# Kernel tuning notes

Measured on AMD Instinct MI355X. Metric: run time of the kernel, lower is better.

The kernel has to match this reference:

```python
import jax, jax.numpy as jnp
import numpy as np
from jax.scipy.linalg import expm

N_WIRES = 9
N_LAYERS = 4
EMBED = 512
BATCH = 64
D = 2 ** N_WIRES
P = N_WIRES * N_LAYERS * 2  # gate angles per sample


def _apply_gate(st, g, w):
    # st: (D, 2,...,2) complex64; apply 2x2 gate g on wire w
    st = jnp.moveaxis(st, 1 + w, -1)
    st = st @ g.T  # new[a] = sum_b g[a,b] old[b]
    return jnp.moveaxis(st, -1, 1 + w)


def _apply_cnot(st, c, t):
    st = jnp.moveaxis(st, (1 + c, 1 + t), (-2, -1))
    st = jnp.concatenate([st[..., 0:1, :], st[..., 1:2, ::-1]], axis=-2)
    return jnp.moveaxis(st, (-2, -1), (1 + c, 1 + t))


def _build_unitary(params):
    # simulate circuit on all D basis states at once (identity input)
    st = jnp.eye(D, dtype=jnp.complex64).reshape((D,) + (2,) * N_WIRES)
    idx = 0
    for _ in range(N_LAYERS):
        for w in range(N_WIRES):
            thy = params[idx]
            thz = params[idx + 1]
            idx += 2
            c = jnp.cos(thy * 0.5).astype(jnp.complex64)
            s = jnp.sin(thy * 0.5).astype(jnp.complex64)
            ry = jnp.stack([jnp.stack([c, -s]), jnp.stack([s, c])])
            ep = jnp.exp(0.5j * thz.astype(jnp.complex64))  # exp(i*thz/2)
            zero = jnp.zeros((), jnp.complex64)
            rz = jnp.stack([jnp.stack([jnp.conj(ep), zero]), jnp.stack([zero, ep])])
            st = _apply_gate(st, rz @ ry, w)  # Ry then Rz, fused
        for w in range(N_WIRES - 1):
            st = _apply_cnot(st, w, w + 1)
        st = _apply_cnot(st, N_WIRES - 1, 0)  # ring entangler (n_wires>1)
    # row index = input basis state i -> column i of U; take real part
    return jnp.real(st.reshape(D, D)).T


def _forward(t, w1, b1, w2, b2):
    h = jax.nn.silu(t[:, None] @ w1 + b1)          # (B, EMBED)
    params = h @ w2 + b2                            # (B, P)
    p_sg = jax.lax.stop_gradient(params)            # torch uses .detach() for the circuit
    U_stack = jax.vmap(_build_unitary)(p_sg)        # (B, D, D)
    B = t.shape[0]
    A = jnp.zeros((B, D * D), params.dtype).at[:, :P].set(params).reshape(B, D, D)
    A_skew = (A - jnp.swapaxes(A, -1, -2)) * 0.01
    U_diff = jax.vmap(expm)(A_skew)                 # (B, D, D)
    return jnp.einsum('bij,bjk->bik', U_stack, U_diff)


def setup_inputs() -> dict:
    key = jax.random.key(0)
    k_t, k1, kb1, k2, kb2 = jax.random.split(key, 5)
    t = jax.random.normal(k_t, (BATCH,), jnp.float32)
    w1 = jax.random.normal(k1, (1, EMBED), jnp.float32)
    b1 = jax.random.normal(kb1, (EMBED,), jnp.float32) * 0.1
    w2 = jax.random.normal(k2, (EMBED, P), jnp.float32) / np.sqrt(EMBED)
    b2 = jax.random.normal(kb2, (P,), jnp.float32) * 0.1
    return {"t": t, "w1": w1, "b1": b1, "w2": w2, "b2": b2}


def reference(t, w1, b1, w2, b2):
    return _forward(t, w1, b1, w2, b2)
```

## Files before the change

### kernel.cpp

```cpp
#include <hip/hip_runtime.h>
#include <math.h>


#define PSTRIDE 2560
#define GD_OFF  0
#define SC_OFF  144
#define L_OFF(l) (160 + (l)*256)
#define V_OFF   1184
#define W_OFF   1280
#define C0_OFF  1792

__device__ __forceinline__ float2 cmul(float2 a, float2 b){
  return make_float2(fmaf(a.x, b.x, -a.y*b.y), fmaf(a.x, b.y, a.y*b.x));
}

__device__ __forceinline__ float2 pk_fma_s_lo(float2 s2, float2 b, float2 c){
  float2 d;
  asm("v_pk_fma_f32 %0, %1, %2, %3 op_sel:[0,0,0] op_sel_hi:[0,1,1]"
      : "=v"(d) : "s"(s2), "v"(b), "v"(c));
  return d;
}
__device__ __forceinline__ float2 pk_mul_s_hi(float2 s2, float2 b){
  float2 d;
  asm("v_pk_mul_f32 %0, %1, %2 op_sel:[1,0] op_sel_hi:[1,1]"
      : "=v"(d) : "s"(s2), "v"(b));
  return d;
}
__device__ __forceinline__ float2 pk_fma_vs_lo(float2 a, float2 b, float2 c){
  float2 d;
  asm("v_pk_fma_f32 %0, %1, %2, %3 op_sel:[0,0,0] op_sel_hi:[0,1,1]"
      : "=v"(d) : "v"(a), "s"(b), "v"(c));
  return d;
}
__device__ __forceinline__ float2 pk_mul_vs_hi(float2 a, float2 b){
  float2 d;
  asm("v_pk_mul_f32 %0, %1, %2 op_sel:[1,0] op_sel_hi:[1,1]"
      : "=v"(d) : "v"(a), "s"(b));
  return d;
}
__device__ __forceinline__ float2 pk_fma_vv_lo(float2 a, float2 b, float2 c){
  float2 d;
  asm("v_pk_fma_f32 %0, %1, %2, %3 op_sel:[0,0,0] op_sel_hi:[0,1,1]"
      : "=v"(d) : "v"(a), "v"(b), "v"(c));
  return d;
}
__device__ __forceinline__ float2 pk_mul_vv_hi(float2 a, float2 b){
  float2 d;
  asm("v_pk_mul_f32 %0, %1, %2 op_sel:[1,0] op_sel_hi:[1,1]"
      : "=v"(d) : "v"(a), "v"(b));
  return d;
}
__device__ __forceinline__ float2 pk_swapneg(float2 c, float2 n){
  float2 d;
  asm("v_pk_mul_f32 %0, %1, %2 op_sel:[1,0] op_sel_hi:[0,1]"
      : "=v"(d) : "v"(c), "v"(n));
  return d;
}

__device__ __forceinline__ int Fperm(int x){
  int S = x ^ (x >> 1); S ^= S >> 2; S ^= S >> 4; S ^= S >> 8;
  return (S & 0xFF) | ((((x >> 8) ^ S) & 1) << 8);
}
__device__ __forceinline__ int physmap(int x){ return x ^ ((x >> 4) & 15); }

template<int STRIDE, bool UNIF>
__device__ __forceinline__ void apply_rot(float2 amp[8], const float* rp){
  const float2 R0 = ((const float2*)rp)[0];
  const float2 R1 = ((const float2*)rp)[1];
  #pragma unroll
  for (int b = 0; b < 8; ++b){
    if (b & STRIDE) continue;
    const float2 u = amp[b], v = amp[b + STRIDE];
    if constexpr (UNIF){
      amp[b]          = pk_fma_s_lo(R0, u, pk_mul_s_hi(R0, v));
      amp[b + STRIDE] = pk_fma_s_lo(R1, u, pk_mul_s_hi(R1, v));
    } else {
      amp[b]          = pk_fma_vv_lo(R0, u, pk_mul_vv_hi(R0, v));
      amp[b + STRIDE] = pk_fma_vv_lo(R1, u, pk_mul_vv_hi(R1, v));
    }
  }
}

template<bool UNIF>
__device__ __forceinline__ void run_layer(float2* __restrict__ S,
    const float* __restrict__ lb, const int lane,
    const int base1, const int base2, const int base3, const int baseF,
    const float2 NEG1P1){
  float2 amp[8];
  #pragma unroll
  for (int j = 0; j < 8; ++j) amp[j] = S[base1 ^ j];
  apply_rot<4, UNIF>(amp, lb + 6*4);
  apply_rot<2, UNIF>(amp, lb + 7*4);
  apply_rot<1, UNIF>(amp, lb + 8*4);
  #pragma unroll
  for (int j = 0; j < 8; ++j) S[base1 ^ j] = amp[j];
  #pragma unroll
  for (int j = 0; j < 8; ++j) amp[j] = S[base2 ^ ((j << 3) ^ (j >> 1))];
  apply_rot<4, UNIF>(amp, lb + 3*4);
  apply_rot<2, UNIF>(amp, lb + 4*4);
  apply_rot<1, UNIF>(amp, lb + 5*4);
  #pragma unroll
  for (int j = 0; j < 8; ++j) S[base2 ^ ((j << 3) ^ (j >> 1))] = amp[j];
  #pragma unroll
  for (int j = 0; j < 8; ++j) amp[j] = S[base3 ^ ((j << 6) ^ ((4*j) & 15))];
  apply_rot<4, UNIF>(amp, lb + 0*4);
  apply_rot<2, UNIF>(amp, lb + 1*4);
  apply_rot<1, UNIF>(amp, lb + 2*4);
  {
    const float2 A  = *(const float2*)(lb + 128 + lane*2);
    const float2 A2 = pk_swapneg(A, NEG1P1);
    #pragma unroll
    for (int j = 0; j < 8; ++j)
      amp[j] = pk_fma_vv_lo(amp[j], A, pk_mul_vv_hi(amp[j], A2));
    #pragma unroll
    for (int j = 0; j < 8; ++j){
      const float2 P = *(const float2*)(lb + 64 + j*4);
      const float2 Q = *(const float2*)(lb + 64 + j*4 + 2);
      if constexpr (UNIF)
        amp[j] = pk_fma_vs_lo(amp[j], P, pk_mul_vs_hi(amp[j], Q));
      else
        amp[j] = pk_fma_vv_lo(amp[j], P, pk_mul_vv_hi(amp[j], Q));
    }
  }
  #pragma unroll
  for (int j = 0; j < 8; ++j) S[baseF ^ physmap(Fperm(j << 6))] = amp[j];
}

__global__ __launch_bounds__(576)
void prep_kernel(const float* __restrict__ t,  const float* __restrict__ w1,
                 const float* __restrict__ b1, const float* __restrict__ w2,
                 const float* __restrict__ b2, float* __restrict__ prep){
  __shared__ float sh[512];
  __shared__ float part[8][72];
  __shared__ float spar[72];
  __shared__ float tl[4][256];
  __shared__ float ssc[3];
  __shared__ __align__(16) float2 vst[2][512];
  const int s = blockIdx.x;
  const float ts = t[s];
  for (int k = threadIdx.x; k < 512; k += 576){
    const float z = fmaf(ts, w1[k], b1[k]);
    sh[k] = z / (1.f + expf(-z));
  }
  __syncthreads();
  {
    const int p = threadIdx.x % 72, c = threadIdx.x / 72;
    float acc = 0.f;
    const int k0 = c*64;
    for (int k = k0; k < k0 + 64; ++k) acc = fmaf(sh[k], w2[k*72 + p], acc);
    part[c][p] = acc;
  }
  __syncthreads();
  if (threadIdx.x < 72){
    const int p = threadIdx.x;
    float acc = b2[p];
    #pragma unroll
    for (int c = 0; c < 8; ++c) acc += part[c][p];
    spar[p] = acc;
  }
  __syncthreads();
  float* pb = prep + (size_t)s*PSTRIDE;
  const int tid = threadIdx.x;
  if (tid < 256){
    const int l = tid >> 6, m = tid & 63;
    float2 acc = make_float2(1.f, 0.f);
    #pragma unroll
    for (int w = 3; w < 9; ++w){
      const float thz = spar[2*(9*l + w) + 1];
      float zi, zr; sincosf(0.5f*thz, &zi, &zr);
      const int bit = (m >> (8 - w)) & 1;
      acc = cmul(acc, make_float2(zr, bit ? zi : -zi));
    }
    pb[L_OFF(l) + 128 + 2*m]     = acc.x;
    pb[L_OFF(l) + 128 + 2*m + 1] = acc.y;
    tl[l][128 + 2*m]     = acc.x;
    tl[l][128 + 2*m + 1] = acc.y;
  } else if (tid < 288){
    const int q = tid - 256, l = q >> 3, j = q & 7;
    float2 acc = make_float2(1.f, 0.f);
    #pragma unroll
    for (int w = 0; w < 3; ++w){
      const float thz = spar[2*(9*l + w) + 1];
      float zi, zr; sincosf(0.5f*thz, &zi, &zr);
      const int bit = (j >> (2 - w)) & 1;
      acc = cmul(acc, make_float2(zr, bit ? zi : -zi));
    }
    float* o = pb + L_OFF(l) + 64 + j*4;
    o[0] = acc.x; o[1] = acc.y; o[2] = -acc.y; o[3] = acc.x;
    float* o2 = &tl[l][64 + j*4];
    o2[0] = acc.x; o2[1] = acc.y; o2[2] = -acc.y; o2[3] = acc.x;
  } else if (tid < 324){
    const int q = tid - 288, l = q / 9, w = q - l*9;
    const float thy = spar[2*(9*l + w)];
    float sy, cy; sincosf(0.5f*thy, &sy, &cy);
    float* o = pb + L_OFF(l) + w*4;
    o[0] = cy; o[1] = -sy; o[2] = sy; o[3] = cy;
    float* o2 = &tl[l][w*4];
    o2[0] = cy; o2[1] = -sy; o2[2] = sy; o2[3] = cy;
  } else if (tid < 333){
    const int w = tid - 324;
    const float thy = spar[2*w], thz = spar[2*w + 1];
    float sy, cy, zi, zr;
    sincosf(0.5f*thy, &sy, &cy);
    sincosf(0.5f*thz, &zi, &zr);
    const float gr[4] = { zr*cy, -zr*sy, zr*sy, zr*cy };
    const float gi[4] = { -zi*cy, zi*sy, zi*sy, zi*cy };
    float* o = pb + GD_OFF + w*16;
    #pragma unroll
    for (int e = 0; e < 4; ++e){
      o[e*4+0] = gr[e]; o[e*4+1] = gi[e]; o[e*4+2] = -gi[e]; o[e*4+3] = gr[e];
    }
  } else if (tid < 405){
    const int j = tid - 333;
    pb[V_OFF + j] = (j == 0) ? 0.f : 0.01f*spar[j];
  } else if (tid == 405){
    float th2 = 0.f;
    for (int j = 1; j < 72; ++j){ const float v = 0.01f*spar[j]; th2 = fmaf(v, v, th2); }
    const float th = sqrtf(th2);
    float alpha, beta;
    if (th > 1e-6f){
      alpha = sinf(th)/th;
      const float s2 = sinf(0.5f*th);
      beta = 2.f*s2*s2/th2;
    } else { alpha = 1.f - th2/6.f; beta = 0.5f; }
    pb[SC_OFF+0] = cosf(th);
    pb[SC_OFF+1] = alpha;
    pb[SC_OFF+2] = beta;
    ssc[0] = cosf(th); ssc[1] = alpha; ssc[2] = beta;
  }
  __syncthreads();
  if (tid < 128){
    const int wv = tid >> 6, lane = tid & 63;
    float2* const S = vst[wv];
    const float2 NEG1P1 = make_float2(-1.f, 1.f);
    const int base1 = (lane << 3) ^ ((lane >> 1) & 15);
    const int hq = lane >> 3, lq = lane & 7;
    const int base2 = (hq << 6) ^ ((hq << 2) & 15) ^ lq;
    const int base3 = lane ^ (lane >> 4);
    const int baseF = physmap(Fperm(lane));
    #pragma unroll
    for (int j = 0; j < 8; ++j){
      const int x = (lane << 3) + j;
      float re;
      if (wv == 0) re = (x == 0) ? 1.f : 0.f;
      else         re = (x >= 1 && x < 72) ? 0.01f*spar[x] : 0.f;
      S[base1 ^ j] = make_float2(re, 0.f);
    }
    #pragma unroll
    for (int L = 0; L < 4; ++L)
      run_layer<false>(S, &tl[L][0], lane, base1, base2, base3, baseF, NEG1P1);
  }
  __syncthreads();
  if (tid < 512){
    const int a  = tid;
    const int pa = a ^ ((a >> 4) & 15);
    const float u0 = vst[0][pa].x;
    const float uv = vst[1][pa].x;
    pb[W_OFF  + a] = fmaf(ssc[1], u0, -ssc[2]*uv);
    pb[C0_OFF + a] = fmaf(ssc[0], u0, -ssc[1]*uv);
  }
}

__global__ __launch_bounds__(512, 6)
void sim_kernel(const float* __restrict__ prep, float* __restrict__ out){
  __shared__ __align__(16) float2 st[8][512];
  const int s    = blockIdx.x & 63;
  const int cb   = blockIdx.x >> 6;
  const int wid  = threadIdx.x >> 6;
  const int lane = threadIdx.x & 63;
  const int col  = cb*8 + wid;
  const float* gp = prep + (size_t)s*PSTRIDE;
  float2* const S = st[wid];
  const float2 NEG1P1 = make_float2(-1.f, 1.f);

  float2 amp[8];
  {
    float2 base = make_float2(1.f, 0.f);
    #pragma unroll
    for (int w = 0; w < 6; ++w){
      const int xb = (lane >> (5 - w)) & 1;
      const int ib = (col  >> (8 - w)) & 1;
      const float4 gd = *(const float4*)(gp + GD_OFF + w*16 + (xb*2 + ib)*4);
      const float2 d1 = make_float2(gd.x, gd.y);
      const float2 d2 = make_float2(gd.z, gd.w);
      base = pk_fma_vv_lo(base, d1, pk_mul_vv_hi(base, d2));
    }
    const int i6 = (col >> 2) & 1, i7 = (col >> 1) & 1, i8 = col & 1;
    float2 g6[2]; float4 g7d[2], g8d[2];
    #pragma unroll
    for (int r = 0; r < 2; ++r){
      g6[r]  = *(const float2*)(gp + GD_OFF + 6*16 + (r*2 + i6)*4);
      g7d[r] = *(const float4*)(gp + GD_OFF + 7*16 + (r*2 + i7)*4);
      g8d[r] = *(const float4*)(gp + GD_OFF + 8*16 + (r*2 + i8)*4);
    }
    float2 g67[4];
    #pragma unroll
    for (int a = 0; a < 2; ++a){
      #pragma unroll
      for (int b = 0; b < 2; ++b){
        const float2 d1 = make_float2(g7d[b].x, g7d[b].y);
        const float2 d2 = make_float2(g7d[b].z, g7d[b].w);
        g67[a*2+b] = pk_fma_vv_lo(g6[a], d1, pk_mul_vv_hi(g6[a], d2));
      }
    }
    const float2 bd2 = pk_swapneg(base, NEG1P1);
    #pragma unroll
    for (int j = 0; j < 8; ++j){
      const float4 g8 = g8d[j & 1];
      const float2 e1 = make_float2(g8.x, g8.y);
      const float2 e2 = make_float2(g8.z, g8.w);
      const float2 T  = pk_fma_vv_lo(g67[j >> 1], e1, pk_mul_vv_hi(g67[j >> 1], e2));
      amp[j] = pk_fma_vv_lo(T, base, pk_mul_vv_hi(T, bd2));
    }
    const int bFI = physmap(Fperm(lane << 3));
    #pragma unroll
    for (int j = 0; j < 8; ++j) S[bFI ^ physmap(Fperm(j))] = amp[j];
  }

  const int base1 = (lane << 3) ^ ((lane >> 1) & 15);
  const int hq = lane >> 3, lq = lane & 7;
  const int base2 = (hq << 6) ^ ((hq << 2) & 15) ^ lq;
  const int base3 = lane ^ (lane >> 4);
  const int baseF = physmap(Fperm(lane));

  run_layer<true>(S, gp + L_OFF(1), lane, base1, base2, base3, baseF, NEG1P1);
  run_layer<true>(S, gp + L_OFF(2), lane, base1, base2, base3, baseF, NEG1P1);
  run_layer<true>(S, gp + L_OFF(3), lane, base1, base2, base3, baseF, NEG1P1);

  __syncthreads();
  const float* wt  = gp + W_OFF;
  const float* c0t = gp + C0_OFF;
  const float* vt  = gp + V_OFF;
  #pragma unroll
  for (int rep = 0; rep < 2; ++rep){
    const int a  = (threadIdx.x >> 1) + rep*256;
    const int q  = threadIdx.x & 1;
    const int pa = a ^ ((a >> 4) & 15);
    float4 vv;
    vv.x = st[q*4 + 0][pa].x;
    vv.y = st[q*4 + 1][pa].x;
    vv.z = st[q*4 + 2][pa].x;
    vv.w = st[q*4 + 3][pa].x;
    if (cb < 9){
      const float  wa = wt[a];
      const float4 vj = *(const float4*)(vt + cb*8 + q*4);
      vv.x = fmaf(wa, vj.x, vv.x);
      vv.y = fmaf(wa, vj.y, vv.y);
      vv.z = fmaf(wa, vj.z, vv.z);
      vv.w = fmaf(wa, vj.w, vv.w);
      if ((cb | q) == 0) vv.x = c0t[a];
    }
    *(float4*)&out[(size_t)s*262144 + (size_t)a*512 + cb*8 + q*4] = vv;
  }
}

extern "C" void kernel_launch(void* const* d_in, const int* in_sizes, int n_in,
                              void* d_out, int out_size, void* d_ws, size_t ws_size,
                              hipStream_t stream){
  const float* t  = (const float*)d_in[0];
  const float* w1 = (const float*)d_in[1];
  const float* b1 = (const float*)d_in[2];
  const float* w2 = (const float*)d_in[3];
  const float* b2 = (const float*)d_in[4];
  float* out  = (float*)d_out;
  float* prep = (float*)d_ws;
  prep_kernel<<<64,   576, 0, stream>>>(t, w1, b1, w2, b2, prep);
  sim_kernel <<<4096, 512, 0, stream>>>(prep, out);
}
```

Before: 144.2 us.

## Apply middle-wire rotations via cross-lane DPP/swizzle instead of LDS round trip

```diff
diff --git a/kernel.cpp b/kernel.cpp
--- a/kernel.cpp
+++ b/kernel.cpp
@@ -26,6 +26,12 @@
       : "=v"(d) : "s"(s2), "v"(b));
   return d;
 }
+__device__ __forceinline__ float2 pk_mul_s_lo(float2 s2, float2 b){
+  float2 d;
+  asm("v_pk_mul_f32 %0, %1, %2 op_sel:[0,0] op_sel_hi:[0,1]"
+      : "=v"(d) : "s"(s2), "v"(b));
+  return d;
+}
 __device__ __forceinline__ float2 pk_fma_vs_lo(float2 a, float2 b, float2 c){
   float2 d;
   asm("v_pk_fma_f32 %0, %1, %2, %3 op_sel:[0,0,0] op_sel_hi:[0,1,1]"
@@ -55,6 +61,19 @@
   asm("v_pk_mul_f32 %0, %1, %2 op_sel:[1,0] op_sel_hi:[0,1]"
       : "=v"(d) : "v"(c), "v"(n));
   return d;
+}
+
+template<int OFS>
+__device__ __forceinline__ float2 swz2(float2 v){
+  const int x = __builtin_amdgcn_ds_swizzle(__float_as_int(v.x), OFS);
+  const int y = __builtin_amdgcn_ds_swizzle(__float_as_int(v.y), OFS);
+  return make_float2(__int_as_float(x), __int_as_float(y));
+}
+template<int CTRL>
+__device__ __forceinline__ float2 dpp2(float2 v){
+  const int x = __builtin_amdgcn_mov_dpp(__float_as_int(v.x), CTRL, 0xF, 0xF, true);
+  const int y = __builtin_amdgcn_mov_dpp(__float_as_int(v.y), CTRL, 0xF, 0xF, true);
+  return make_float2(__int_as_float(x), __int_as_float(y));
 }
 
 __device__ __forceinline__ int Fperm(int x){
@@ -81,31 +100,30 @@
   }
 }
 
-template<bool UNIF>
-__device__ __forceinline__ void run_layer(float2* __restrict__ S,
+__device__ __forceinline__ void run_layer2(float2* __restrict__ S,
     const float* __restrict__ lb, const int lane,
     const int base1, const int base2, const int base3, const int baseF,
     const float2 NEG1P1){
   float2 amp[8];
   #pragma unroll
   for (int j = 0; j < 8; ++j) amp[j] = S[base1 ^ j];
-  apply_rot<4, UNIF>(amp, lb + 6*4);
-  apply_rot<2, UNIF>(amp, lb + 7*4);
-  apply_rot<1, UNIF>(amp, lb + 8*4);
+  apply_rot<4,false>(amp, lb + 6*4);
+  apply_rot<2,false>(amp, lb + 7*4);
+  apply_rot<1,false>(amp, lb + 8*4);
   #pragma unroll
   for (int j = 0; j < 8; ++j) S[base1 ^ j] = amp[j];
   #pragma unroll
   for (int j = 0; j < 8; ++j) amp[j] = S[base2 ^ ((j << 3) ^ (j >> 1))];
-  apply_rot<4, UNIF>(amp, lb + 3*4);
-  apply_rot<2, UNIF>(amp, lb + 4*4);
-  apply_rot<1, UNIF>(amp, lb + 5*4);
+  apply_rot<4,false>(amp, lb + 3*4);
+  apply_rot<2,false>(amp, lb + 4*4);
+  apply_rot<1,false>(amp, lb + 5*4);
   #pragma unroll
   for (int j = 0; j < 8; ++j) S[base2 ^ ((j << 3) ^ (j >> 1))] = amp[j];
   #pragma unroll
   for (int j = 0; j < 8; ++j) amp[j] = S[base3 ^ ((j << 6) ^ ((4*j) & 15))];
-  apply_rot<4, UNIF>(amp, lb + 0*4);
-  apply_rot<2, UNIF>(amp, lb + 1*4);
-  apply_rot<1, UNIF>(amp, lb + 2*4);
+  apply_rot<4,false>(amp, lb + 0*4);
+  apply_rot<2,false>(amp, lb + 1*4);
+  apply_rot<1,false>(amp, lb + 2*4);
   {
     const float2 A  = *(const float2*)(lb + 128 + lane*2);
     const float2 A2 = pk_swapneg(A, NEG1P1);
@@ -116,10 +134,56 @@
     for (int j = 0; j < 8; ++j){
       const float2 P = *(const float2*)(lb + 64 + j*4);
       const float2 Q = *(const float2*)(lb + 64 + j*4 + 2);
-      if constexpr (UNIF)
-        amp[j] = pk_fma_vs_lo(amp[j], P, pk_mul_vs_hi(amp[j], Q));
-      else
-        amp[j] = pk_fma_vv_lo(amp[j], P, pk_mul_vv_hi(amp[j], Q));
+      amp[j] = pk_fma_vv_lo(amp[j], P, pk_mul_vv_hi(amp[j], Q));
+    }
+  }
+  #pragma unroll
+  for (int j = 0; j < 8; ++j) S[baseF ^ physmap(Fperm(j << 6))] = amp[j];
+}
+
+#define XROT(GET, RP, BIT) {                                        \
+    const float2 R0 = ((const float2*)(RP))[0];    \
+    const float2 R1 = ((const float2*)(RP))[1];    \
+    const float  Bs = (BIT) ? R1.x : R0.y;                          \
+    const float2 Bv = make_float2(Bs, Bs);                          \
+    _Pragma("unroll")                                               \
+    for (int j = 0; j < 8; ++j){                                    \
+      const float2 p = GET(amp[j]);                                 \
+      amp[j] = pk_fma_vv_lo(Bv, p, pk_mul_s_lo(R0, amp[j]));        \
+    }                                                               \
+  }
+
+__device__ __forceinline__ void run_layer_h(float2* __restrict__ S,
+    const float* __restrict__ lb, const int lane,
+    const int base1, const int base3, const int baseF,
+    const float2 NEG1P1){
+  float2 amp[8];
+  #pragma unroll
+  for (int j = 0; j < 8; ++j) amp[j] = S[base1 ^ j];
+  apply_rot<4,true>(amp, lb + 6*4);
+  apply_rot<2,true>(amp, lb + 7*4);
+  apply_rot<1,true>(amp, lb + 8*4);
+  XROT(swz2<0x101F>, lb + 3*4, (lane >> 2) & 1);
+  XROT(dpp2<0x4E>,   lb + 4*4, (lane >> 1) & 1);
+  XROT(dpp2<0xB1>,   lb + 5*4, lane & 1);
+  #pragma unroll
+  for (int j = 0; j < 8; ++j) S[base1 ^ j] = amp[j];
+  #pragma unroll
+  for (int j = 0; j < 8; ++j) amp[j] = S[base3 ^ ((j << 6) ^ ((4*j) & 15))];
+  apply_rot<4,true>(amp, lb + 0*4);
+  apply_rot<2,true>(amp, lb + 1*4);
+  apply_rot<1,true>(amp, lb + 2*4);
+  {
+    const float2 A  = *(const float2*)(lb + 128 + lane*2);
+    const float2 A2 = pk_swapneg(A, NEG1P1);
+    #pragma unroll
+    for (int j = 0; j < 8; ++j)
+      amp[j] = pk_fma_vv_lo(amp[j], A, pk_mul_vv_hi(amp[j], A2));
+    #pragma unroll
+    for (int j = 0; j < 8; ++j){
+      const float2 P = *(const float2*)(lb + 64 + j*4);
+      const float2 Q = *(const float2*)(lb + 64 + j*4 + 2);
+      amp[j] = pk_fma_vs_lo(amp[j], P, pk_mul_vs_hi(amp[j], Q));
     }
   }
   #pragma unroll
@@ -248,7 +312,7 @@
     }
     #pragma unroll
     for (int L = 0; L < 4; ++L)
-      run_layer<false>(S, &tl[L][0], lane, base1, base2, base3, baseF, NEG1P1);
+      run_layer2(S, &tl[L][0], lane, base1, base2, base3, baseF, NEG1P1);
   }
   __syncthreads();
   if (tid < 512){
@@ -318,14 +382,12 @@
   }
 
   const int base1 = (lane << 3) ^ ((lane >> 1) & 15);
-  const int hq = lane >> 3, lq = lane & 7;
-  const int base2 = (hq << 6) ^ ((hq << 2) & 15) ^ lq;
   const int base3 = lane ^ (lane >> 4);
   const int baseF = physmap(Fperm(lane));
 
-  run_layer<true>(S, gp + L_OFF(1), lane, base1, base2, base3, baseF, NEG1P1);
-  run_layer<true>(S, gp + L_OFF(2), lane, base1, base2, base3, baseF, NEG1P1);
-  run_layer<true>(S, gp + L_OFF(3), lane, base1, base2, base3, baseF, NEG1P1);
+  run_layer_h(S, gp + L_OFF(1), lane, base1, base3, baseF, NEG1P1);
+  run_layer_h(S, gp + L_OFF(2), lane, base1, base3, baseF, NEG1P1);
+  run_layer_h(S, gp + L_OFF(3), lane, base1, base3, baseF, NEG1P1);
 
   __syncthreads();
   const float* wt  = gp + W_OFF;
```

Measured after the change: 143.2 us, median of 3. No clear change (-0.7%).
